# Kernel optimization log

Hardware: AMD Instinct MI355X
Metric: run time of the kernel (lower is better)

The kernel has to match this reference:

```python
import jax, jax.numpy as jnp
import numpy as np

N_NODES = 50000
N_EDGES = 800000
MUL = 32            # multiplicity of 0e and 1o feature irreps
N_SPECIES = 4       # node_attr = 4x0e one-hot
N_BASIS = 8         # radial basis scalars
N_HID = 8           # invariant_neurons
AVG_NEIGH = 16.0
INV_SQRT3 = 1.0 / np.sqrt(3.0).astype(np.float32)


def setup_inputs() -> dict:
    key = jax.random.key(0)
    ks = jax.random.split(key, 16)
    x = jax.random.normal(ks[0], (N_NODES, MUL * 4), jnp.float32)  # 32x0e + 32x1o
    species = jax.random.randint(ks[1], (N_NODES,), 0, N_SPECIES)
    node_attr = jax.nn.one_hot(species, N_SPECIES, dtype=jnp.float32)
    edge_embedding = jax.random.normal(ks[2], (N_EDGES, N_BASIS), jnp.float32)
    edge_attr = jax.random.normal(ks[3], (N_EDGES, 4), jnp.float32)  # 1x0e + 1x1o
    edge_index = jax.random.randint(ks[4], (2, N_EDGES), 0, N_NODES)
    # learned params
    W_lin1_s = jax.random.normal(ks[5], (MUL, MUL), jnp.float32)
    W_lin1_v = jax.random.normal(ks[6], (MUL, MUL), jnp.float32)
    fc_w1 = jax.random.normal(ks[7], (N_BASIS, N_HID), jnp.float32)
    fc_w2 = jax.random.normal(ks[8], (N_HID, 4 * MUL), jnp.float32)  # tp.weight_numel = 4*MUL
    W_lin2_s = jax.random.normal(ks[9], (2 * MUL, MUL), jnp.float32)  # mid simplify: 64x0e
    W_lin2_v = jax.random.normal(ks[10], (2 * MUL, MUL), jnp.float32)  # 64x1o
    W_sc_s = jax.random.normal(ks[11], (MUL, N_SPECIES, MUL), jnp.float32)
    W_sc_v = jax.random.normal(ks[12], (MUL, N_SPECIES, MUL), jnp.float32)
    return dict(node_features=x, node_attr=node_attr, edge_embedding=edge_embedding,
                edge_attr=edge_attr, edge_index=edge_index,
                W_lin1_s=W_lin1_s, W_lin1_v=W_lin1_v, fc_w1=fc_w1, fc_w2=fc_w2,
                W_lin2_s=W_lin2_s, W_lin2_v=W_lin2_v, W_sc_s=W_sc_s, W_sc_v=W_sc_v)


def _forward(node_features, node_attr, edge_embedding, edge_attr, edge_index,
             W_lin1_s, W_lin1_v, fc_w1, fc_w2, W_lin2_s, W_lin2_v, W_sc_s, W_sc_v):
    n = node_features.shape[0]
    xs = node_features[:, :MUL]                       # [N, 32] scalars (0e)
    xv = node_features[:, MUL:].reshape(n, MUL, 3)    # [N, 32, 3] vectors (1o)

    # self-connection: FullyConnectedTensorProduct(feat, 4x0e -> feat), uvw weights
    sc_norm = 1.0 / np.sqrt(MUL * N_SPECIES).astype(np.float32)
    sc_s = jnp.einsum('nu,nv,uvw->nw', xs, node_attr, W_sc_s) * sc_norm
    sc_v = jnp.einsum('nui,nv,uvw->nwi', xv, node_attr, W_sc_v) * sc_norm

    # linear_1: per-irrep channel mixing, 1/sqrt(fan_in)
    l1n = 1.0 / np.sqrt(MUL).astype(np.float32)
    ys = (xs @ W_lin1_s) * l1n
    yv = jnp.einsum('nui,uw->nwi', xv, W_lin1_v) * l1n

    # radial MLP -> per-edge tensor-product weights (4 paths x MUL)
    h = jax.nn.silu((edge_embedding @ fc_w1) / np.sqrt(N_BASIS).astype(np.float32))
    w = (h @ fc_w2) / np.sqrt(N_HID).astype(np.float32)  # [E, 128]
    w00, w01, w10, w11 = jnp.split(w, 4, axis=1)          # instruction order (0,0),(0,1),(1,0),(1,1)

    src = edge_index[0]
    dst = edge_index[1]
    es = ys[src]                                          # [E, 32]
    ev = yv[src]                                          # [E, 32, 3]
    a0 = edge_attr[:, 0]                                  # [E]    0e
    a1 = edge_attr[:, 1:4]                                # [E, 3] 1o

    # per-edge weighted uvu tensor product paths
    o_s_a = w00 * es * a0[:, None]                                       # 0e x 0e -> 0e
    o_s_b = w11 * jnp.einsum('eui,ei->eu', ev, a1) * INV_SQRT3           # 1o x 1o -> 0e
    o_v_a = (w01 * es)[:, :, None] * a1[:, None, :]                      # 0e x 1o -> 1o
    o_v_b = w10[:, :, None] * ev * a0[:, None, None]                     # 1o x 0e -> 1o

    # scatter-sum to destination nodes
    mid_s = jax.ops.segment_sum(jnp.concatenate([o_s_a, o_s_b], axis=1), dst, num_segments=n)
    mid_v = jax.ops.segment_sum(jnp.concatenate([o_v_a, o_v_b], axis=1), dst, num_segments=n)
    inv = 1.0 / np.sqrt(AVG_NEIGH).astype(np.float32)
    mid_s = mid_s * inv   # [N, 64]
    mid_v = mid_v * inv   # [N, 64, 3]

    # linear_2: 64x0e+64x1o -> 32x0e+32x1o
    l2n = 1.0 / np.sqrt(2 * MUL).astype(np.float32)
    out_s = (mid_s @ W_lin2_s) * l2n + sc_s
    out_v = jnp.einsum('nui,uw->nwi', mid_v, W_lin2_v) * l2n + sc_v
    return jnp.concatenate([out_s, out_v.reshape(n, MUL * 3)], axis=1)


def reference(node_features, node_attr, edge_embedding, edge_attr, edge_index,
              W_lin1_s, W_lin1_v, fc_w1, fc_w2, W_lin2_s, W_lin2_v, W_sc_s, W_sc_v):
    return _forward(node_features, node_attr, edge_embedding, edge_attr, edge_index,
                    W_lin1_s, W_lin1_v, fc_w1, fc_w2, W_lin2_s, W_lin2_v, W_sc_s, W_sc_v)
```

## Files before the change

kernel.cpp:

```cpp
#include <hip/hip_runtime.h>
#include <hip/hip_bf16.h>

#define N_NODES 50000
#define N_EDGES 800000
#define CAP 48
#define CSTRIDE 16
#define NODE_BLOCKS 1250
#define BUCKET_BLOCKS 1563

__device__ __forceinline__ unsigned short f2bf(float f) {
    union { float f; unsigned u; } t; t.f = f;
    unsigned r = t.u + 0x7FFF + ((t.u >> 16) & 1);
    return (unsigned short)(r >> 16);
}

__global__ __launch_bounds__(256) void prep_kernel(
    const float* __restrict__ x, const float* __restrict__ attr,
    const float* __restrict__ W1s, const float* __restrict__ W1v,
    const float* __restrict__ Wscs, const float* __restrict__ Wscv,
    const int* __restrict__ eidx,
    int* __restrict__ counts, int* __restrict__ bucket,
    unsigned short* __restrict__ ysvh, float* __restrict__ out)
{
    __shared__ float shm[2048];
    const int tid = threadIdx.x;

    if (blockIdx.x < NODE_BLOCKS) {
        const int nl = tid >> 5;
        const int w  = tid & 31;

        float w1s[32], w1v[32];
        #pragma unroll
        for (int u = 0; u < 32; ++u) {
            w1s[u] = W1s[u*32 + w];
            w1v[u] = W1v[u*32 + w];
        }

        const float l1n = 0.17677669529663687f;
        const float scn = 0.08838834764831843f;

        for (int batch = 0; batch < 5; ++batch) {
            const int node0 = blockIdx.x * 40 + batch * 8;
            float* xbuf = shm + (batch & 1) * 1024;
            ((float4*)xbuf)[tid] = ((const float4*)(x + (long)node0 * 128))[tid];
            __syncthreads();

            const int node = node0 + nl;
            const float* at = attr + (long)node * 4;
            int sp = 0;
            if (at[1] > 0.5f) sp = 1;
            if (at[2] > 0.5f) sp = 2;
            if (at[3] > 0.5f) sp = 3;

            const float* lx   = xbuf + nl * 128;
            const float* gscs = Wscs + sp * 32 + w;
            const float* gscv = Wscv + sp * 32 + w;

            float ys = 0.f, yv0 = 0.f, yv1 = 0.f, yv2 = 0.f;
            float ss = 0.f, sv0 = 0.f, sv1 = 0.f, sv2 = 0.f;
            #pragma unroll
            for (int u4 = 0; u4 < 8; ++u4) {
                const float4 xs4 = ((const float4*)lx)[u4];
                const float4 q0  = ((const float4*)(lx + 32))[u4*3 + 0];
                const float4 q1  = ((const float4*)(lx + 32))[u4*3 + 1];
                const float4 q2  = ((const float4*)(lx + 32))[u4*3 + 2];
                const float xsv[4]  = {xs4.x, xs4.y, xs4.z, xs4.w};
                const float xvv[12] = {q0.x,q0.y,q0.z,q0.w,
                                       q1.x,q1.y,q1.z,q1.w,
                                       q2.x,q2.y,q2.z,q2.w};
                #pragma unroll
                for (int j = 0; j < 4; ++j) {
                    const int u = u4*4 + j;
                    const float wss = gscs[u*128];
                    const float wsv = gscv[u*128];
                    ys  += xsv[j] * w1s[u];
                    yv0 += xvv[3*j+0] * w1v[u];
                    yv1 += xvv[3*j+1] * w1v[u];
                    yv2 += xvv[3*j+2] * w1v[u];
                    ss  += xsv[j] * wss;
                    sv0 += xvv[3*j+0] * wsv;
                    sv1 += xvv[3*j+1] * wsv;
                    sv2 += xvv[3*j+2] * wsv;
                }
            }

            uint2 pk;
            pk.x = (unsigned)f2bf(ys  * l1n) | ((unsigned)f2bf(yv0 * l1n) << 16);
            pk.y = (unsigned)f2bf(yv1 * l1n) | ((unsigned)f2bf(yv2 * l1n) << 16);
            *(uint2*)(ysvh + (long)node * 128 + w * 4) = pk;

            float* op = out + (long)node * 128;
            op[w] = ss * scn;
            op[32 + 3*w + 0] = sv0 * scn;
            op[32 + 3*w + 1] = sv1 * scn;
            op[32 + 3*w + 2] = sv2 * scn;
        }
    } else {
        const int gid = (blockIdx.x - NODE_BLOCKS) * 256 + tid;
        if (gid < N_EDGES/2) {
            const int d0 = eidx[N_EDGES + gid];
            const int d1 = eidx[N_EDGES + gid + N_EDGES/2];
            const int s0 = atomicAdd(&counts[d0 * CSTRIDE], 1);
            const int s1 = atomicAdd(&counts[d1 * CSTRIDE], 1);
            if (s0 < CAP) bucket[(long)d0 * CAP + s0] = gid;
            if (s1 < CAP) bucket[(long)d1 * CAP + s1] = gid + N_EDGES/2;
        }
    }
}

__global__ __launch_bounds__(256) void agg_kernel(
    const float* __restrict__ ee, const float* __restrict__ eattr,
    const int* __restrict__ eidx,
    const float* __restrict__ fcw1, const float* __restrict__ fcw2,
    const float* __restrict__ W2s, const float* __restrict__ W2v,
    const unsigned short* __restrict__ ysvh,
    const int* __restrict__ counts, const int* __restrict__ bucket,
    float* __restrict__ out)
{
    __shared__ float hrec[8][32 * 12];
    __shared__ float mid[8][256];

    const int tid = threadIdx.x;
    const int nl = tid >> 5;
    const int u  = tid & 31;
    const int node = blockIdx.x * 8 + nl;
    const float inv_sqrt8 = 0.35355339059327373f;

    float f2r[8][4];
    #pragma unroll
    for (int j = 0; j < 8; ++j) {
        f2r[j][0] = fcw2[j*128 + u];
        f2r[j][1] = fcw2[j*128 + 32 + u];
        f2r[j][2] = fcw2[j*128 + 64 + u];
        f2r[j][3] = fcw2[j*128 + 96 + u];
    }

    const int cnt = min(counts[node * CSTRIDE], CAP);
    int e0 = bucket[(long)node * CAP + min(u, CAP-1)];
    const bool dummy = (u >= cnt);
    if (dummy) e0 = 0;
    const int s0 = dummy ? 0 : eidx[e0];

    {
        const float4 ea = ((const float4*)(ee + (long)e0 * 8))[0];
        const float4 eb = ((const float4*)(ee + (long)e0 * 8))[1];
        const float4 at = ((const float4*)eattr)[e0];
        const float eev[8] = {ea.x, ea.y, ea.z, ea.w, eb.x, eb.y, eb.z, eb.w};
        float* hr = hrec[nl] + u * 12;
        float h[8];
        #pragma unroll
        for (int j = 0; j < 8; ++j) {
            float pre = 0.f;
            #pragma unroll
            for (int b = 0; b < 8; ++b) pre += eev[b] * fcw1[b*8 + j];
            pre *= inv_sqrt8;
            const float s = pre / (1.f + __expf(-pre)) * inv_sqrt8;
            h[j] = dummy ? 0.f : s;
        }
        ((float4*)hr)[0] = make_float4(h[0], h[1], h[2], h[3]);
        ((float4*)hr)[1] = make_float4(h[4], h[5], h[6], h[7]);
        ((float4*)hr)[2] = at;
    }

    float msa = 0.f, msb = 0.f;
    float va0 = 0.f, va1 = 0.f, va2 = 0.f;
    float vb0 = 0.f, vb1 = 0.f, vb2 = 0.f;

    #define ACCUM(HA, HB, AT, Y)                                             \
    {                                                                        \
        const float es = __uint_as_float((Y).x << 16);                       \
        const float ex = __uint_as_float((Y).x & 0xffff0000u);               \
        const float ey = __uint_as_float((Y).y << 16);                       \
        const float ez = __uint_as_float((Y).y & 0xffff0000u);               \
        const float hh[8] = {HA.x,HA.y,HA.z,HA.w,HB.x,HB.y,HB.z,HB.w};       \
        float w00=0.f, w01=0.f, w10=0.f, w11=0.f;                            \
        _Pragma("unroll")                                                    \
        for (int j = 0; j < 8; ++j) {                                        \
            w00 += hh[j]*f2r[j][0]; w01 += hh[j]*f2r[j][1];                  \
            w10 += hh[j]*f2r[j][2]; w11 += hh[j]*f2r[j][3];                  \
        }                                                                    \
        const float a0 = AT.x, a1x = AT.y, a1y = AT.z, a1z = AT.w;           \
        msa += w00 * es * a0;                                                \
        msb += w11 * (ex*a1x + ey*a1y + ez*a1z);                             \
        const float t = w01 * es;                                            \
        va0 += t*a1x; va1 += t*a1y; va2 += t*a1z;                            \
        const float s = w10 * a0;                                            \
        vb0 += s*ex; vb1 += s*ey; vb2 += s*ez;                               \
    }

    #define GATHER(SLOT) \
        (*(const uint2*)(ysvh + (long)__shfl(s0, (SLOT), 32) * 128 + u * 4))

    const int c0 = min(cnt, 32);
    {
        uint2 y0 = GATHER(0), y1 = GATHER(1), y2 = GATHER(2), y3 = GATHER(3);
        for (int k = 0; k < c0; k += 4) {
            const int kn = (k + 4) & 31;
            const uint2 n0 = GATHER(kn);
            const uint2 n1 = GATHER(kn + 1);
            const uint2 n2 = GATHER(kn + 2);
            const uint2 n3 = GATHER(kn + 3);
            const float4* h0p = (const float4*)(hrec[nl] + (k + 0) * 12);
            const float4* h1p = (const float4*)(hrec[nl] + (k + 1) * 12);
            const float4* h2p = (const float4*)(hrec[nl] + (k + 2) * 12);
            const float4* h3p = (const float4*)(hrec[nl] + (k + 3) * 12);
            const float4 A0 = h0p[0], B0 = h0p[1], T0 = h0p[2];
            const float4 A1 = h1p[0], B1 = h1p[1], T1 = h1p[2];
            const float4 A2 = h2p[0], B2 = h2p[1], T2 = h2p[2];
            const float4 A3 = h3p[0], B3 = h3p[1], T3 = h3p[2];
            ACCUM(A0, B0, T0, y0)
            ACCUM(A1, B1, T1, y1)
            ACCUM(A2, B2, T2, y2)
            ACCUM(A3, B3, T3, y3)
            y0 = n0; y1 = n1; y2 = n2; y3 = n3;
        }
    }

    if (cnt > 32) {
        int be = bucket[(long)node * CAP + min(32 + u, CAP-1)];
        if (32 + u >= cnt) be = 0;
        for (int k = 32; k < cnt; ++k) {
            const int e = __shfl(be, k - 32, 32);
            const int s = eidx[e];
            const float4 ea = ((const float4*)(ee + (long)e * 8))[0];
            const float4 eb = ((const float4*)(ee + (long)e * 8))[1];
            const float4 at = ((const float4*)eattr)[e];
            const float eev[8] = {ea.x, ea.y, ea.z, ea.w, eb.x, eb.y, eb.z, eb.w};
            float h[8];
            #pragma unroll
            for (int j = 0; j < 8; ++j) {
                float pre = 0.f;
                #pragma unroll
                for (int b = 0; b < 8; ++b) pre += eev[b] * fcw1[b*8 + j];
                pre *= inv_sqrt8;
                h[j] = pre / (1.f + __expf(-pre)) * inv_sqrt8;
            }
            const float4 HA = make_float4(h[0], h[1], h[2], h[3]);
            const float4 HB = make_float4(h[4], h[5], h[6], h[7]);
            const uint2 y = *(const uint2*)(ysvh + (long)s * 128 + u * 4);
            ACCUM(HA, HB, at, y)
        }
    }
    #undef GATHER
    #undef ACCUM

    msb *= 0.5773502691896258f;

    float* m = mid[nl];
    m[u]       = msa;
    m[32 + u]  = msb;
    m[64  + u*3 + 0] = va0;  m[64  + u*3 + 1] = va1;  m[64  + u*3 + 2] = va2;
    m[160 + u*3 + 0] = vb0;  m[160 + u*3 + 1] = vb1;  m[160 + u*3 + 2] = vb2;

    float os = 0.f, ov0 = 0.f, ov1 = 0.f, ov2 = 0.f;
    #pragma unroll 8
    for (int q = 0; q < 32; ++q) {
        const float wsa = W2s[q*32 + u];
        const float wsb = W2s[(32 + q)*32 + u];
        os += m[q] * wsa + m[32 + q] * wsb;
        const float wva = W2v[q*32 + u];
        const float wvb = W2v[(32 + q)*32 + u];
        ov0 += m[64 + q*3 + 0] * wva + m[160 + q*3 + 0] * wvb;
        ov1 += m[64 + q*3 + 1] * wva + m[160 + q*3 + 1] * wvb;
        ov2 += m[64 + q*3 + 2] * wva + m[160 + q*3 + 2] * wvb;
    }

    const float sc = 0.03125f;
    float* op = out + (long)node * 128;
    op[u]            += os  * sc;
    op[32 + 3*u + 0] += ov0 * sc;
    op[32 + 3*u + 1] += ov1 * sc;
    op[32 + 3*u + 2] += ov2 * sc;
}

extern "C" void kernel_launch(void* const* d_in, const int* in_sizes, int n_in,
                              void* d_out, int out_size, void* d_ws, size_t ws_size,
                              hipStream_t stream) {
    const float* x     = (const float*)d_in[0];
    const float* attr  = (const float*)d_in[1];
    const float* ee    = (const float*)d_in[2];
    const float* eattr = (const float*)d_in[3];
    const int*   eidx  = (const int*)  d_in[4];
    const float* W1s   = (const float*)d_in[5];
    const float* W1v   = (const float*)d_in[6];
    const float* fcw1  = (const float*)d_in[7];
    const float* fcw2  = (const float*)d_in[8];
    const float* W2s   = (const float*)d_in[9];
    const float* W2v   = (const float*)d_in[10];
    const float* Wscs  = (const float*)d_in[11];
    const float* Wscv  = (const float*)d_in[12];

    float* out = (float*)d_out;

    unsigned short* ysvh = (unsigned short*)d_ws;
    int*   counts = (int*)(ysvh + (long)N_NODES * 128);
    int*   bucket = counts + (long)N_NODES * CSTRIDE;

    hipMemsetAsync(counts, 0, (long)N_NODES * CSTRIDE * sizeof(int), stream);
    prep_kernel<<<NODE_BLOCKS + BUCKET_BLOCKS, 256, 0, stream>>>(
        x, attr, W1s, W1v, Wscs, Wscv, eidx, counts, bucket, ysvh, out);
    agg_kernel<<<N_NODES/8, 256, 0, stream>>>(ee, eattr, eidx, fcw1, fcw2,
                                              W2s, W2v, ysvh, counts, bucket, out);
}
```

Measured before the change: 289.7 us.

## Simplify prep kernel: one node-octet per block, one edge per thread, dense counts

Node blocks now each process 8 nodes, reading x directly from global memory instead of staging five batches through shared memory. Edge bucketing uses one edge per thread instead of two. The counts array drops its 16-int padding stride, so the memset shrinks and count reads become dense. The intent is more parallelism and fewer memset bytes. The cost is more contention on the now-adjacent atomic counters, reloading the W1 weights per 8 nodes, and uncoalesced per-thread x reads.

New measurement: 338.7 us. 16.9% more time.

```diff
diff --git a/kernel.cpp b/kernel.cpp
--- a/kernel.cpp
+++ b/kernel.cpp
@@ -4,9 +4,8 @@
 #define N_NODES 50000
 #define N_EDGES 800000
 #define CAP 48
-#define CSTRIDE 16
-#define NODE_BLOCKS 1250
-#define BUCKET_BLOCKS 1563
+#define NODE_BLOCKS 6250
+#define BUCKET_BLOCKS (N_EDGES/256)
 
 __device__ __forceinline__ unsigned short f2bf(float f) {
     union { float f; unsigned u; } t; t.f = f;
@@ -22,12 +21,12 @@
     int* __restrict__ counts, int* __restrict__ bucket,
     unsigned short* __restrict__ ysvh, float* __restrict__ out)
 {
-    __shared__ float shm[2048];
     const int tid = threadIdx.x;
 
     if (blockIdx.x < NODE_BLOCKS) {
         const int nl = tid >> 5;
         const int w  = tid & 31;
+        const int node = blockIdx.x * 8 + nl;
 
         float w1s[32], w1v[32];
         #pragma unroll
@@ -36,75 +35,62 @@
             w1v[u] = W1v[u*32 + w];
         }
 
+        const float* at = attr + (long)node * 4;
+        int sp = 0;
+        if (at[1] > 0.5f) sp = 1;
+        if (at[2] > 0.5f) sp = 2;
+        if (at[3] > 0.5f) sp = 3;
+
+        const float4* xr   = (const float4*)(x + (long)node * 128);
+        const float*  gscs = Wscs + sp * 32 + w;
+        const float*  gscv = Wscv + sp * 32 + w;
+
         const float l1n = 0.17677669529663687f;
         const float scn = 0.08838834764831843f;
 
-        for (int batch = 0; batch < 5; ++batch) {
-            const int node0 = blockIdx.x * 40 + batch * 8;
-            float* xbuf = shm + (batch & 1) * 1024;
-            ((float4*)xbuf)[tid] = ((const float4*)(x + (long)node0 * 128))[tid];
-            __syncthreads();
-
-            const int node = node0 + nl;
-            const float* at = attr + (long)node * 4;
-            int sp = 0;
-            if (at[1] > 0.5f) sp = 1;
-            if (at[2] > 0.5f) sp = 2;
-            if (at[3] > 0.5f) sp = 3;
-
-            const float* lx   = xbuf + nl * 128;
-            const float* gscs = Wscs + sp * 32 + w;
-            const float* gscv = Wscv + sp * 32 + w;
-
-            float ys = 0.f, yv0 = 0.f, yv1 = 0.f, yv2 = 0.f;
-            float ss = 0.f, sv0 = 0.f, sv1 = 0.f, sv2 = 0.f;
+        float ys = 0.f, yv0 = 0.f, yv1 = 0.f, yv2 = 0.f;
+        float ss = 0.f, sv0 = 0.f, sv1 = 0.f, sv2 = 0.f;
+        #pragma unroll
+        for (int u4 = 0; u4 < 8; ++u4) {
+            const float4 xs4 = xr[u4];
+            const float4 q0  = xr[8 + u4*3 + 0];
+            const float4 q1  = xr[8 + u4*3 + 1];
+            const float4 q2  = xr[8 + u4*3 + 2];
+            const float xsv[4]  = {xs4.x, xs4.y, xs4.z, xs4.w};
+            const float xvv[12] = {q0.x,q0.y,q0.z,q0.w,
+                                   q1.x,q1.y,q1.z,q1.w,
+                                   q2.x,q2.y,q2.z,q2.w};
             #pragma unroll
-            for (int u4 = 0; u4 < 8; ++u4) {
-                const float4 xs4 = ((const float4*)lx)[u4];
-                const float4 q0  = ((const float4*)(lx + 32))[u4*3 + 0];
-                const float4 q1  = ((const float4*)(lx + 32))[u4*3 + 1];
-                const float4 q2  = ((const float4*)(lx + 32))[u4*3 + 2];
-                const float xsv[4]  = {xs4.x, xs4.y, xs4.z, xs4.w};
-                const float xvv[12] = {q0.x,q0.y,q0.z,q0.w,
-                                       q1.x,q1.y,q1.z,q1.w,
-                                       q2.x,q2.y,q2.z,q2.w};
-                #pragma unroll
-                for (int j = 0; j < 4; ++j) {
-                    const int u = u4*4 + j;
-                    const float wss = gscs[u*128];
-                    const float wsv = gscv[u*128];
-                    ys  += xsv[j] * w1s[u];
-                    yv0 += xvv[3*j+0] * w1v[u];
-                    yv1 += xvv[3*j+1] * w1v[u];
-                    yv2 += xvv[3*j+2] * w1v[u];
-                    ss  += xsv[j] * wss;
-                    sv0 += xvv[3*j+0] * wsv;
-                    sv1 += xvv[3*j+1] * wsv;
-                    sv2 += xvv[3*j+2] * wsv;
-                }
+            for (int j = 0; j < 4; ++j) {
+                const int u = u4*4 + j;
+                const float wss = gscs[u*128];
+                const float wsv = gscv[u*128];
+                ys  += xsv[j] * w1s[u];
+                yv0 += xvv[3*j+0] * w1v[u];
+                yv1 += xvv[3*j+1] * w1v[u];
+                yv2 += xvv[3*j+2] * w1v[u];
+                ss  += xsv[j] * wss;
+                sv0 += xvv[3*j+0] * wsv;
+                sv1 += xvv[3*j+1] * wsv;
+                sv2 += xvv[3*j+2] * wsv;
             }
-
-            uint2 pk;
-            pk.x = (unsigned)f2bf(ys  * l1n) | ((unsigned)f2bf(yv0 * l1n) << 16);
-            pk.y = (unsigned)f2bf(yv1 * l1n) | ((unsigned)f2bf(yv2 * l1n) << 16);
-            *(uint2*)(ysvh + (long)node * 128 + w * 4) = pk;
-
-            float* op = out + (long)node * 128;
-            op[w] = ss * scn;
-            op[32 + 3*w + 0] = sv0 * scn;
-            op[32 + 3*w + 1] = sv1 * scn;
-            op[32 + 3*w + 2] = sv2 * scn;
-        }
+        }
+
+        uint2 pk;
+        pk.x = (unsigned)f2bf(ys  * l1n) | ((unsigned)f2bf(yv0 * l1n) << 16);
+        pk.y = (unsigned)f2bf(yv1 * l1n) | ((unsigned)f2bf(yv2 * l1n) << 16);
+        *(uint2*)(ysvh + (long)node * 128 + w * 4) = pk;
+
+        float* op = out + (long)node * 128;
+        op[w] = ss * scn;
+        op[32 + 3*w + 0] = sv0 * scn;
+        op[32 + 3*w + 1] = sv1 * scn;
+        op[32 + 3*w + 2] = sv2 * scn;
     } else {
-        const int gid = (blockIdx.x - NODE_BLOCKS) * 256 + tid;
-        if (gid < N_EDGES/2) {
-            const int d0 = eidx[N_EDGES + gid];
-            const int d1 = eidx[N_EDGES + gid + N_EDGES/2];
-            const int s0 = atomicAdd(&counts[d0 * CSTRIDE], 1);
-            const int s1 = atomicAdd(&counts[d1 * CSTRIDE], 1);
-            if (s0 < CAP) bucket[(long)d0 * CAP + s0] = gid;
-            if (s1 < CAP) bucket[(long)d1 * CAP + s1] = gid + N_EDGES/2;
-        }
+        const int e = (blockIdx.x - NODE_BLOCKS) * 256 + tid;
+        const int dst = eidx[N_EDGES + e];
+        const int slot = atomicAdd(&counts[dst], 1);
+        if (slot < CAP) bucket[(long)dst * CAP + slot] = e;
     }
 }
 
@@ -135,8 +121,8 @@
         f2r[j][3] = fcw2[j*128 + 96 + u];
     }
 
-    const int cnt = min(counts[node * CSTRIDE], CAP);
-    int e0 = bucket[(long)node * CAP + min(u, CAP-1)];
+    const int cnt = min(counts[node], CAP);
+    int e0 = bucket[(long)node * CAP + u];
     const bool dummy = (u >= cnt);
     if (dummy) e0 = 0;
     const int s0 = dummy ? 0 : eidx[e0];
@@ -294,9 +280,9 @@
 
     unsigned short* ysvh = (unsigned short*)d_ws;
     int*   counts = (int*)(ysvh + (long)N_NODES * 128);
-    int*   bucket = counts + (long)N_NODES * CSTRIDE;
-
-    hipMemsetAsync(counts, 0, (long)N_NODES * CSTRIDE * sizeof(int), stream);
+    int*   bucket = counts + N_NODES;
+
+    hipMemsetAsync(counts, 0, N_NODES * sizeof(int), stream);
     prep_kernel<<<NODE_BLOCKS + BUCKET_BLOCKS, 256, 0, stream>>>(
         x, attr, W1s, W1v, Wscs, Wscv, eidx, counts, bucket, ysvh, out);
     agg_kernel<<<N_NODES/8, 256, 0, stream>>>(ee, eattr, eidx, fcw1, fcw2,
```
